# Performance work log

Measured on AMD Instinct MI355X. Metric: run time of the kernel, lower is better.

## Reference

```python
import jax, jax.numpy as jnp
import numpy as np

B, T, P = 4096, 128, 2
D_m = D_g = D_p = D_e = 256


def gru_cell(x, h, w_ih, w_hh, b_ih, b_hh):
    # PyTorch GRUCell math
    gi = x @ w_ih.T + b_ih          # [N, 3H]
    gh = h @ w_hh.T + b_hh          # [N, 3H]
    ir, iz, inn = jnp.split(gi, 3, axis=1)
    hr, hz, hn = jnp.split(gh, 3, axis=1)
    r = jax.nn.sigmoid(ir + hr)
    z = jax.nn.sigmoid(iz + hz)
    n = jnp.tanh(inn + r * hn)
    return (1.0 - z) * n + z * h


def _gru_params(key, in_dim, hid):
    k1, k2, k3, k4 = jax.random.split(key, 4)
    s = 1.0 / np.sqrt(hid)
    u = lambda k, shp: jax.random.uniform(k, shp, jnp.float32, -s, s)
    return u(k1, (3 * hid, in_dim)), u(k2, (3 * hid, hid)), u(k3, (3 * hid,)), u(k4, (3 * hid,))


def setup_inputs() -> dict:
    key = jax.random.key(0)
    ks = jax.random.split(key, 10)
    U = jax.random.normal(ks[0], (B, D_m), jnp.float32)
    qm_idx = jax.random.randint(ks[1], (B,), 0, P)
    g_hist = jax.random.normal(ks[2], (T, B, D_g), jnp.float32)
    q0 = jax.random.normal(ks[3], (B, P, D_p), jnp.float32)
    e0 = jax.random.normal(ks[4], (B, D_e), jnp.float32)
    wg = _gru_params(ks[5], D_m + D_p, D_g)
    wp = _gru_params(ks[6], D_m + D_g, D_p)
    we = _gru_params(ks[7], D_p, D_e)
    sa = 1.0 / np.sqrt(D_g)
    attn_w = jax.random.uniform(ks[8], (1, D_g), jnp.float32, -sa, sa)
    return {
        "U": U, "qm_idx": qm_idx, "g_hist": g_hist, "q0": q0, "e0": e0,
        "wg_ih": wg[0], "wg_hh": wg[1], "bg_ih": wg[2], "bg_hh": wg[3],
        "wp_ih": wp[0], "wp_hh": wp[1], "bp_ih": wp[2], "bp_hh": wp[3],
        "we_ih": we[0], "we_hh": we[1], "be_ih": we[2], "be_hh": we[3],
        "attn_w": attn_w,
    }


def reference(U, qm_idx, g_hist, q0, e0,
              wg_ih, wg_hh, bg_ih, bg_hh,
              wp_ih, wp_hh, bp_ih, bp_hh,
              we_ih, we_hh, be_ih, be_hh,
              attn_w):
    b_idx = jnp.arange(U.shape[0])
    qmask = jax.nn.one_hot(qm_idx, P, dtype=U.dtype)             # [B, P]
    # _select_parties: gather the speaking party's state
    q0_sel = q0[b_idx, qm_idx]                                    # [B, D_p]
    # global GRU step (g_hist non-empty -> hidden = g_hist[-1])
    g_ = gru_cell(jnp.concatenate([U, q0_sel], axis=1), g_hist[-1],
                  wg_ih, wg_hh, bg_ih, bg_hh)                     # [B, D_g]
    # SimpleAttention over history: softmax over time of a scalar score
    scale = jnp.einsum('tbd,od->tb', g_hist, attn_w)              # [T, B]
    alpha_t = jax.nn.softmax(scale, axis=0)                       # [T, B]
    c_ = jnp.einsum('tb,tbd->bd', alpha_t, g_hist)                # [B, D_g]
    alpha = alpha_t.T[:, None, :]                                 # [B, 1, T]
    # party GRU applied to every party slot
    U_c = jnp.concatenate([U, c_], axis=1)                        # [B, D_m+D_g]
    U_c_exp = jnp.broadcast_to(U_c[:, None, :], (U.shape[0], P, U_c.shape[1]))
    qs_ = gru_cell(U_c_exp.reshape(-1, D_m + D_g), q0.reshape(-1, D_p),
                   wp_ih, wp_hh, bp_ih, bp_hh).reshape(U.shape[0], P, D_p)
    # listener_state=False: listeners keep q0; speaker slot takes qs_
    qm = qmask[..., None]
    q_ = q0 * (1.0 - qm) + qs_ * qm                               # [B, P, D_p]
    # emotion GRU on the speaking party's updated state
    e_ = gru_cell(q_[b_idx, qm_idx], e0, we_ih, we_hh, be_ih, be_hh)  # [B, D_e]
    return g_, q_, e_, alpha
```

## Files before the change

### kernel.cpp

```cpp
#include <hip/hip_runtime.h>
#include <hip/hip_bf16.h>
#include <cstdint>
#include <cstddef>

#define B_N   4096
#define T_N   128
#define P_N   2
#define D     256
#define NG    768
#define BD    (B_N * D)
#define AGRID 1024
#define AGSIZE (AGRID * 256)

typedef __attribute__((ext_vector_type(4))) float f32x4;
typedef __attribute__((ext_vector_type(8))) short bf16x8;
typedef __attribute__((ext_vector_type(8))) unsigned short ushort8;

__device__ __forceinline__ unsigned short f2bf(float f) {
    __hip_bfloat16 h = __float2bfloat16(f);
    return *reinterpret_cast<unsigned short*>(&h);
}

struct AttnParams {
    const float *U, *g_hist, *q0, *e0;
    const int   *qm;
    const float *wg_ih, *wg_hh, *wp_ih, *wp_hh, *we_ih, *we_hh;
    const float *attn_w;
    float *a_out;
    unsigned short *U_bf, *e0_bf, *glast_bf, *q0sel_bf, *c_bf;
    unsigned short *wgih_bf, *wpih_bf, *wghh_bf, *wphh_bf, *weih_bf, *wehh_bf;
};

struct GPParams {
    const unsigned short *U_bf, *q0sel_bf, *glast_bf, *c_bf;
    const unsigned short *wgih_bf, *wghh_bf, *wpih_bf, *wphh_bf;
    const float *bg_ih, *bg_hh, *bp_ih, *bp_hh;
    const float *g_last, *q0;
    const int *qm;
    float *g_out, *q_out;
    unsigned short *qssel_bf;
};

__device__ __forceinline__ void cvt8(
    const float* __restrict__ src, unsigned short* __restrict__ dst,
    int n8, int gtid)
{
    for (int i = gtid; i < n8; i += AGSIZE) {
        const float4* s = reinterpret_cast<const float4*>(src + i * 8);
        const float4 v0 = s[0], v1 = s[1];
        ushort8 o = { f2bf(v0.x), f2bf(v0.y), f2bf(v0.z), f2bf(v0.w),
                      f2bf(v1.x), f2bf(v1.y), f2bf(v1.z), f2bf(v1.w) };
        *reinterpret_cast<ushort8*>(dst + i * 8) = o;
    }
}

__global__ __launch_bounds__(256) void attn_fused(AttnParams p)
{
    const int tid  = threadIdx.x;
    const int lane = tid & 63;
    const int wid  = tid >> 6;
    const int gtid = blockIdx.x * 256 + tid;

    const float* g_last = p.g_hist + (size_t)(T_N - 1) * BD;

    cvt8(p.wg_ih, p.wgih_bf, NG * 512 / 8, gtid);
    cvt8(p.wg_hh, p.wghh_bf, NG * 256 / 8, gtid);
    cvt8(p.wp_ih, p.wpih_bf, NG * 512 / 8, gtid);
    cvt8(p.wp_hh, p.wphh_bf, NG * 256 / 8, gtid);
    cvt8(p.we_ih, p.weih_bf, NG * 256 / 8, gtid);
    cvt8(p.we_hh, p.wehh_bf, NG * 256 / 8, gtid);
    cvt8(p.U,     p.U_bf,     B_N * D / 8, gtid);
    cvt8(p.e0,    p.e0_bf,    B_N * D / 8, gtid);
    cvt8(g_last,  p.glast_bf, B_N * D / 8, gtid);
    for (int i = gtid; i < B_N * D / 4; i += AGSIZE) {
        const int row = i >> 6;
        const int j   = (i & 63) * 4;
        const float4 v = *reinterpret_cast<const float4*>(
            p.q0 + ((size_t)row * P_N + p.qm[row]) * D + j);
        ushort4 bv = { f2bf(v.x), f2bf(v.y), f2bf(v.z), f2bf(v.w) };
        *reinterpret_cast<ushort4*>(p.q0sel_bf + (size_t)row * D + j) = bv;
    }

    const int b = blockIdx.x * 4 + wid;

    const float4 w4 = *reinterpret_cast<const float4*>(p.attn_w + lane * 4);
    const float* gbase = p.g_hist + (size_t)b * D + lane * 4;

    float  m = -INFINITY, l = 0.f;
    float4 acc = {0.f, 0.f, 0.f, 0.f};
    float  s0 = 0.f, s1 = 0.f;

    auto step = [&](int t, const float4& g) {
        float dot = g.x * w4.x + g.y * w4.y + g.z * w4.z + g.w * w4.w;
        #pragma unroll
        for (int off = 32; off >= 1; off >>= 1)
            dot += __shfl_xor(dot, off, 64);
        const float mn   = fmaxf(m, dot);
        const float corr = __expf(m - mn);
        const float pr   = __expf(dot - mn);
        l = l * corr + pr;
        acc.x = fmaf(pr, g.x, acc.x * corr);
        acc.y = fmaf(pr, g.y, acc.y * corr);
        acc.z = fmaf(pr, g.z, acc.z * corr);
        acc.w = fmaf(pr, g.w, acc.w * corr);
        m = mn;
        if ((t & 63) == lane) { if (t & 64) s1 = dot; else s0 = dot; }
    };

    for (int t = 0; t < T_N; t += 2) {
        const float4 g0 = *reinterpret_cast<const float4*>(gbase + (size_t)t * BD);
        const float4 g1 = *reinterpret_cast<const float4*>(gbase + (size_t)(t + 1) * BD);
        step(t, g0);
        step(t + 1, g1);
    }

    const float rl = 1.f / l;
    ushort4 cv = { f2bf(acc.x * rl), f2bf(acc.y * rl),
                   f2bf(acc.z * rl), f2bf(acc.w * rl) };
    *reinterpret_cast<ushort4*>(p.c_bf + (size_t)b * D + lane * 4) = cv;
    p.a_out[(size_t)b * T_N + lane]      = __expf(s0 - m) * rl;
    p.a_out[(size_t)b * T_N + 64 + lane] = __expf(s1 - m) * rl;
}

template<int MODE, int NI, int LDWI>
__device__ __forceinline__ void gru_body(
    int r0, int c0, unsigned short* smem, int tid,
    const unsigned short* __restrict__ A0,
    const unsigned short* __restrict__ A1,
    const unsigned short* __restrict__ Wi, const float* __restrict__ bi,
    const unsigned short* __restrict__ Ah,
    const unsigned short* __restrict__ Wh, const float* __restrict__ bh,
    const float* __restrict__ hsrc, const int* __restrict__ qm,
    float* __restrict__ out_f32, unsigned short* __restrict__ out_bf)
{
    constexpr int NT = NI + 8;

    const int lane = tid & 63;
    const int wid  = tid >> 6;
    const int st_row = lane >> 2;
    const int st_p   = lane & 3;

    f32x4 accI[2][6] = {};
    f32x4 accH[2][6] = {};

    auto stage = [&](int step, int buf) {
        const unsigned short* Apart;
        const unsigned short* W;
        int kcolA, kcolW, ldw;
        if (step < NI) {
            const int kt = step * 32;
            Apart = (kt < D) ? A0 : A1;
            kcolA = kt & (D - 1);
            kcolW = kt;
            W     = Wi;
            ldw   = LDWI;
        } else {
            const int kt = (step - NI) * 32;
            Apart = Ah; kcolA = kt; kcolW = kt; W = Wh; ldw = D;
        }
        unsigned short* As = smem + buf * 8192;
        unsigned short* Ws = As + 4096;
        #pragma unroll
        for (int c = 0; c < 2; ++c) {
            const int row  = wid * 32 + c * 16 + st_row;
            const int scol = (st_p ^ ((row >> 1) & 3)) * 8;
            __builtin_amdgcn_global_load_lds(
                (const __attribute__((address_space(1))) void*)
                    (Apart + (size_t)(r0 + row) * D + kcolA + scol),
                (__attribute__((address_space(3))) void*)
                    (As + wid * 1024 + c * 512), 16, 0, 0);
            int grp = row >> 5; if (grp == 3) grp = 2;
            const int wrow = grp * 256 + c0 + (row & 31);
            __builtin_amdgcn_global_load_lds(
                (const __attribute__((address_space(1))) void*)
                    (W + (size_t)wrow * ldw + kcolW + scol),
                (__attribute__((address_space(3))) void*)
                    (Ws + wid * 1024 + c * 512), 16, 0, 0);
        }
    };

    auto compute = [&](int buf, f32x4 (&acc)[2][6]) {
        const unsigned short* As = smem + buf * 8192;
        const unsigned short* Ws = As + 4096;
        const int s  = lane >> 4;
        const int fr = lane & 15;
        bf16x8 a[2], b[6];
        #pragma unroll
        for (int m = 0; m < 2; ++m) {
            const int row = wid * 32 + m * 16 + fr;
            const int ph  = s ^ ((row >> 1) & 3);
            a[m] = *reinterpret_cast<const bf16x8*>(&As[row * 32 + ph * 8]);
        }
        #pragma unroll
        for (int j = 0; j < 6; ++j) {
            const int row = j * 16 + fr;
            const int ph  = s ^ ((row >> 1) & 3);
            b[j] = *reinterpret_cast<const bf16x8*>(&Ws[row * 32 + ph * 8]);
        }
        #pragma unroll
        for (int m = 0; m < 2; ++m)
            #pragma unroll
            for (int j = 0; j < 6; ++j)
                acc[m][j] = __builtin_amdgcn_mfma_f32_16x16x32_bf16(
                    a[m], b[j], acc[m][j], 0, 0, 0);
    };

    stage(0, 0);
    stage(1, 1);

    int cb = 0, ib = 2;
    for (int s = 0; s < NT; ++s) {
        if (s + 2 < NT) stage(s + 2, ib);
        const int rem = NT - 1 - s;
        if (rem >= 2)      asm volatile("s_waitcnt vmcnt(8)" ::: "memory");
        else if (rem == 1) asm volatile("s_waitcnt vmcnt(4)" ::: "memory");
        else               asm volatile("s_waitcnt vmcnt(0)" ::: "memory");
        __builtin_amdgcn_sched_barrier(0);
        __builtin_amdgcn_s_barrier();
        if (s < NI) compute(cb, accI);
        else        compute(cb, accH);
        __builtin_amdgcn_s_barrier();
        cb = (cb == 2) ? 0 : cb + 1;
        ib = (ib == 2) ? 0 : ib + 1;
    }

    const int cr = (lane >> 4) * 4;
    const int cc = lane & 15;
    #pragma unroll
    for (int m = 0; m < 2; ++m) {
        #pragma unroll
        for (int jj = 0; jj < 2; ++jj) {
            const int col = c0 + jj * 16 + cc;
            const float bir = bi[col],       bhr = bh[col];
            const float biz = bi[col + 256], bhz = bh[col + 256];
            const float bin = bi[col + 512], bhn = bh[col + 512];
            #pragma unroll
            for (int q = 0; q < 4; ++q) {
                const int row = r0 + wid * 32 + m * 16 + cr + q;
                const float ir  = accI[m][jj][q]     + bir;
                const float hr  = accH[m][jj][q]     + bhr;
                const float iz  = accI[m][jj + 2][q] + biz;
                const float hz  = accH[m][jj + 2][q] + bhz;
                const float in_ = accI[m][jj + 4][q] + bin;
                const float hn  = accH[m][jj + 4][q] + bhn;
                const float rg = 1.f / (1.f + __expf(-(ir + hr)));
                const float zg = 1.f / (1.f + __expf(-(iz + hz)));
                const float ng = tanhf(in_ + rg * hn);
                if (MODE == 1) {
                    const int p = qm[row];
                    const float hv  = hsrc[(size_t)row * 512 + (size_t)p * 256 + col];
                    const float ov  = hsrc[(size_t)row * 512 + (size_t)(1 - p) * 256 + col];
                    const float val = (1.f - zg) * ng + zg * hv;
                    out_f32[(size_t)row * 512 + (size_t)p * 256 + col]       = val;
                    out_f32[(size_t)row * 512 + (size_t)(1 - p) * 256 + col] = ov;
                    out_bf[(size_t)row * 256 + col] = f2bf(val);
                } else {
                    const float hv  = hsrc[(size_t)row * 256 + col];
                    const float val = (1.f - zg) * ng + zg * hv;
                    out_f32[(size_t)row * 256 + col] = val;
                }
            }
        }
    }
}

__global__ __launch_bounds__(256) void gp_gru(GPParams p)
{
    __shared__ unsigned short smem[3 * 8192];
    const int tid = threadIdx.x;
    const int bid = blockIdx.x;

    if (bid < 256) {
        const int r0 = (bid & 31) * 128, c0 = (bid >> 5) * 32;
        gru_body<0, 16, 512>(r0, c0, smem, tid,
            p.U_bf, p.q0sel_bf, p.wgih_bf, p.bg_ih,
            p.glast_bf, p.wghh_bf, p.bg_hh,
            p.g_last, nullptr, p.g_out, nullptr);
    } else {
        const int gb = bid - 256;
        const int r0 = (gb & 31) * 128, c0 = (gb >> 5) * 32;
        gru_body<1, 16, 512>(r0, c0, smem, tid,
            p.U_bf, p.c_bf, p.wpih_bf, p.bp_ih,
            p.q0sel_bf, p.wphh_bf, p.bp_hh,
            p.q0, p.qm, p.q_out, p.qssel_bf);
    }
}

__global__ __launch_bounds__(256) void e_gru(
    const unsigned short* __restrict__ qssel_bf,
    const unsigned short* __restrict__ weih_bf, const float* __restrict__ be_ih,
    const unsigned short* __restrict__ e0_bf,
    const unsigned short* __restrict__ wehh_bf, const float* __restrict__ be_hh,
    const float* __restrict__ e0, float* __restrict__ e_out)
{
    __shared__ unsigned short smem[3 * 8192];
    const int tid = threadIdx.x;
    const int bid = blockIdx.x;
    const int r0 = (bid & 31) * 128, c0 = (bid >> 5) * 32;
    gru_body<0, 8, 256>(r0, c0, smem, tid,
        qssel_bf, nullptr, weih_bf, be_ih,
        e0_bf, wehh_bf, be_hh,
        e0, nullptr, e_out, nullptr);
}

extern "C" void kernel_launch(void* const* d_in, const int* in_sizes, int n_in,
                              void* d_out, int out_size, void* d_ws, size_t ws_size,
                              hipStream_t stream)
{
    const float* U      = (const float*)d_in[0];
    const int*   qm     = (const int*)  d_in[1];
    const float* g_hist = (const float*)d_in[2];
    const float* q0     = (const float*)d_in[3];
    const float* e0     = (const float*)d_in[4];
    const float* wg_ih  = (const float*)d_in[5];
    const float* wg_hh  = (const float*)d_in[6];
    const float* bg_ih  = (const float*)d_in[7];
    const float* bg_hh  = (const float*)d_in[8];
    const float* wp_ih  = (const float*)d_in[9];
    const float* wp_hh  = (const float*)d_in[10];
    const float* bp_ih  = (const float*)d_in[11];
    const float* bp_hh  = (const float*)d_in[12];
    const float* we_ih  = (const float*)d_in[13];
    const float* we_hh  = (const float*)d_in[14];
    const float* be_ih  = (const float*)d_in[15];
    const float* be_hh  = (const float*)d_in[16];
    const float* attn_w = (const float*)d_in[17];

    float* out   = (float*)d_out;
    float* g_out = out;
    float* q_out = out + 1048576;
    float* e_out = out + 3145728;
    float* a_out = out + 4194304;

    unsigned short* bf = (unsigned short*)d_ws;
    unsigned short* U_bf     = bf;
    unsigned short* e0_bf    = bf + 1048576;
    unsigned short* glast_bf = bf + 2097152;
    unsigned short* q0sel_bf = bf + 3145728;
    unsigned short* c_bf     = bf + 4194304;
    unsigned short* qssel_bf = bf + 5242880;
    unsigned short* wgih_bf  = bf + 6291456;
    unsigned short* wpih_bf  = bf + 6684672;
    unsigned short* wghh_bf  = bf + 7077888;
    unsigned short* wphh_bf  = bf + 7274496;
    unsigned short* weih_bf  = bf + 7471104;
    unsigned short* wehh_bf  = bf + 7667712;

    const float* g_last = g_hist + (size_t)(T_N - 1) * BD;

    AttnParams ap;
    ap.U = U; ap.g_hist = g_hist; ap.q0 = q0; ap.e0 = e0; ap.qm = qm;
    ap.wg_ih = wg_ih; ap.wg_hh = wg_hh; ap.wp_ih = wp_ih; ap.wp_hh = wp_hh;
    ap.we_ih = we_ih; ap.we_hh = we_hh; ap.attn_w = attn_w;
    ap.a_out = a_out;
    ap.U_bf = U_bf; ap.e0_bf = e0_bf; ap.glast_bf = glast_bf;
    ap.q0sel_bf = q0sel_bf; ap.c_bf = c_bf;
    ap.wgih_bf = wgih_bf; ap.wpih_bf = wpih_bf; ap.wghh_bf = wghh_bf;
    ap.wphh_bf = wphh_bf; ap.weih_bf = weih_bf; ap.wehh_bf = wehh_bf;

    GPParams gp;
    gp.U_bf = U_bf; gp.q0sel_bf = q0sel_bf; gp.glast_bf = glast_bf;
    gp.c_bf = c_bf;
    gp.wgih_bf = wgih_bf; gp.wghh_bf = wghh_bf;
    gp.wpih_bf = wpih_bf; gp.wphh_bf = wphh_bf;
    gp.bg_ih = bg_ih; gp.bg_hh = bg_hh; gp.bp_ih = bp_ih; gp.bp_hh = bp_hh;
    gp.g_last = g_last; gp.q0 = q0; gp.qm = qm;
    gp.g_out = g_out; gp.q_out = q_out; gp.qssel_bf = qssel_bf;

    const dim3 blk(256);
    attn_fused<<<AGRID, blk, 0, stream>>>(ap);
    gp_gru<<<512, blk, 0, stream>>>(gp);
    e_gru<<<256, blk, 0, stream>>>(
        qssel_bf, weih_bf, be_ih, e0_bf, wehh_bf, be_hh, e0, e_out);
}
```

Measured before the change: 162.0 us.

## Replace LDS-staged block GEMM with per-wave register-pipelined GRU tiles

The GRU GEMMs no longer stage A and W tiles through shared memory with block barriers. Each wave now independently computes a 16x32 output tile, loading its A and W fragments straight from global memory into registers with a 4-deep software pipeline. Grids are doubled so there are enough waves to cover the same output. Removing the barriers and LDS traffic trades away data reuse across waves: each W fragment is now fetched by many more waves, so more global/L2 traffic and register pressure.

```diff
diff --git a/kernel.cpp b/kernel.cpp
--- a/kernel.cpp
+++ b/kernel.cpp
@@ -123,8 +123,8 @@
 }
 
 template<int MODE, int NI, int LDWI>
-__device__ __forceinline__ void gru_body(
-    int r0, int c0, unsigned short* smem, int tid,
+__device__ __forceinline__ void gru_wave(
+    int row0, int c0, int lane,
     const unsigned short* __restrict__ A0,
     const unsigned short* __restrict__ A1,
     const unsigned short* __restrict__ Wi, const float* __restrict__ bi,
@@ -135,130 +135,93 @@
 {
     constexpr int NT = NI + 8;
 
-    const int lane = tid & 63;
-    const int wid  = tid >> 6;
-    const int st_row = lane >> 2;
-    const int st_p   = lane & 3;
-
-    f32x4 accI[2][6] = {};
-    f32x4 accH[2][6] = {};
-
-    auto stage = [&](int step, int buf) {
+    const int fr = lane & 15;
+    const int s  = lane >> 4;
+
+    f32x4 accI[6] = {};
+    f32x4 accH[6] = {};
+
+    bf16x8 a[4];
+    bf16x8 b[4][6];
+
+    auto loadstep = [&](int st, int buf) {
         const unsigned short* Apart;
         const unsigned short* W;
         int kcolA, kcolW, ldw;
-        if (step < NI) {
-            const int kt = step * 32;
+        if (st < NI) {
+            const int kt = st * 32;
             Apart = (kt < D) ? A0 : A1;
             kcolA = kt & (D - 1);
             kcolW = kt;
             W     = Wi;
             ldw   = LDWI;
         } else {
-            const int kt = (step - NI) * 32;
+            const int kt = (st - NI) * 32;
             Apart = Ah; kcolA = kt; kcolW = kt; W = Wh; ldw = D;
         }
-        unsigned short* As = smem + buf * 8192;
-        unsigned short* Ws = As + 4096;
+        a[buf] = *reinterpret_cast<const bf16x8*>(
+            Apart + (size_t)(row0 + fr) * D + kcolA + s * 8);
         #pragma unroll
-        for (int c = 0; c < 2; ++c) {
-            const int row  = wid * 32 + c * 16 + st_row;
-            const int scol = (st_p ^ ((row >> 1) & 3)) * 8;
-            __builtin_amdgcn_global_load_lds(
-                (const __attribute__((address_space(1))) void*)
-                    (Apart + (size_t)(r0 + row) * D + kcolA + scol),
-                (__attribute__((address_space(3))) void*)
-                    (As + wid * 1024 + c * 512), 16, 0, 0);
-            int grp = row >> 5; if (grp == 3) grp = 2;
-            const int wrow = grp * 256 + c0 + (row & 31);
-            __builtin_amdgcn_global_load_lds(
-                (const __attribute__((address_space(1))) void*)
-                    (W + (size_t)wrow * ldw + kcolW + scol),
-                (__attribute__((address_space(3))) void*)
-                    (Ws + wid * 1024 + c * 512), 16, 0, 0);
+        for (int j = 0; j < 6; ++j) {
+            const int wrow = (j >> 1) * 256 + c0 + (j & 1) * 16 + fr;
+            b[buf][j] = *reinterpret_cast<const bf16x8*>(
+                W + (size_t)wrow * ldw + kcolW + s * 8);
         }
     };
 
-    auto compute = [&](int buf, f32x4 (&acc)[2][6]) {
-        const unsigned short* As = smem + buf * 8192;
-        const unsigned short* Ws = As + 4096;
-        const int s  = lane >> 4;
-        const int fr = lane & 15;
-        bf16x8 a[2], b[6];
-        #pragma unroll
-        for (int m = 0; m < 2; ++m) {
-            const int row = wid * 32 + m * 16 + fr;
-            const int ph  = s ^ ((row >> 1) & 3);
-            a[m] = *reinterpret_cast<const bf16x8*>(&As[row * 32 + ph * 8]);
-        }
-        #pragma unroll
-        for (int j = 0; j < 6; ++j) {
-            const int row = j * 16 + fr;
-            const int ph  = s ^ ((row >> 1) & 3);
-            b[j] = *reinterpret_cast<const bf16x8*>(&Ws[row * 32 + ph * 8]);
-        }
-        #pragma unroll
-        for (int m = 0; m < 2; ++m)
+    loadstep(0, 0);
+    loadstep(1, 1);
+    loadstep(2, 2);
+
+    #pragma unroll
+    for (int st = 0; st < NT; ++st) {
+        if (st + 3 < NT) loadstep(st + 3, (st + 3) & 3);
+        const int buf = st & 3;
+        if (st < NI) {
             #pragma unroll
             for (int j = 0; j < 6; ++j)
-                acc[m][j] = __builtin_amdgcn_mfma_f32_16x16x32_bf16(
-                    a[m], b[j], acc[m][j], 0, 0, 0);
-    };
-
-    stage(0, 0);
-    stage(1, 1);
-
-    int cb = 0, ib = 2;
-    for (int s = 0; s < NT; ++s) {
-        if (s + 2 < NT) stage(s + 2, ib);
-        const int rem = NT - 1 - s;
-        if (rem >= 2)      asm volatile("s_waitcnt vmcnt(8)" ::: "memory");
-        else if (rem == 1) asm volatile("s_waitcnt vmcnt(4)" ::: "memory");
-        else               asm volatile("s_waitcnt vmcnt(0)" ::: "memory");
-        __builtin_amdgcn_sched_barrier(0);
-        __builtin_amdgcn_s_barrier();
-        if (s < NI) compute(cb, accI);
-        else        compute(cb, accH);
-        __builtin_amdgcn_s_barrier();
-        cb = (cb == 2) ? 0 : cb + 1;
-        ib = (ib == 2) ? 0 : ib + 1;
-    }
-
-    const int cr = (lane >> 4) * 4;
-    const int cc = lane & 15;
+                accI[j] = __builtin_amdgcn_mfma_f32_16x16x32_bf16(
+                    a[buf], b[buf][j], accI[j], 0, 0, 0);
+        } else {
+            #pragma unroll
+            for (int j = 0; j < 6; ++j)
+                accH[j] = __builtin_amdgcn_mfma_f32_16x16x32_bf16(
+                    a[buf], b[buf][j], accH[j], 0, 0, 0);
+        }
+    }
+
+    const int cr = s * 4;
+    const int cc = fr;
     #pragma unroll
-    for (int m = 0; m < 2; ++m) {
+    for (int jj = 0; jj < 2; ++jj) {
+        const int col = c0 + jj * 16 + cc;
+        const float bir = bi[col],       bhr = bh[col];
+        const float biz = bi[col + 256], bhz = bh[col + 256];
+        const float bin = bi[col + 512], bhn = bh[col + 512];
         #pragma unroll
-        for (int jj = 0; jj < 2; ++jj) {
-            const int col = c0 + jj * 16 + cc;
-            const float bir = bi[col],       bhr = bh[col];
-            const float biz = bi[col + 256], bhz = bh[col + 256];
-            const float bin = bi[col + 512], bhn = bh[col + 512];
-            #pragma unroll
-            for (int q = 0; q < 4; ++q) {
-                const int row = r0 + wid * 32 + m * 16 + cr + q;
-                const float ir  = accI[m][jj][q]     + bir;
-                const float hr  = accH[m][jj][q]     + bhr;
-                const float iz  = accI[m][jj + 2][q] + biz;
-                const float hz  = accH[m][jj + 2][q] + bhz;
-                const float in_ = accI[m][jj + 4][q] + bin;
-                const float hn  = accH[m][jj + 4][q] + bhn;
-                const float rg = 1.f / (1.f + __expf(-(ir + hr)));
-                const float zg = 1.f / (1.f + __expf(-(iz + hz)));
-                const float ng = tanhf(in_ + rg * hn);
-                if (MODE == 1) {
-                    const int p = qm[row];
-                    const float hv  = hsrc[(size_t)row * 512 + (size_t)p * 256 + col];
-                    const float ov  = hsrc[(size_t)row * 512 + (size_t)(1 - p) * 256 + col];
-                    const float val = (1.f - zg) * ng + zg * hv;
-                    out_f32[(size_t)row * 512 + (size_t)p * 256 + col]       = val;
-                    out_f32[(size_t)row * 512 + (size_t)(1 - p) * 256 + col] = ov;
-                    out_bf[(size_t)row * 256 + col] = f2bf(val);
-                } else {
-                    const float hv  = hsrc[(size_t)row * 256 + col];
-                    const float val = (1.f - zg) * ng + zg * hv;
-                    out_f32[(size_t)row * 256 + col] = val;
-                }
+        for (int q = 0; q < 4; ++q) {
+            const int row = row0 + cr + q;
+            const float ir  = accI[jj][q]     + bir;
+            const float hr  = accH[jj][q]     + bhr;
+            const float iz  = accI[jj + 2][q] + biz;
+            const float hz  = accH[jj + 2][q] + bhz;
+            const float in_ = accI[jj + 4][q] + bin;
+            const float hn  = accH[jj + 4][q] + bhn;
+            const float rg = 1.f / (1.f + __expf(-(ir + hr)));
+            const float zg = 1.f / (1.f + __expf(-(iz + hz)));
+            const float ng = tanhf(in_ + rg * hn);
+            if (MODE == 1) {
+                const int p = qm[row];
+                const float hv  = hsrc[(size_t)row * 512 + (size_t)p * 256 + col];
+                const float ov  = hsrc[(size_t)row * 512 + (size_t)(1 - p) * 256 + col];
+                const float val = (1.f - zg) * ng + zg * hv;
+                out_f32[(size_t)row * 512 + (size_t)p * 256 + col]       = val;
+                out_f32[(size_t)row * 512 + (size_t)(1 - p) * 256 + col] = ov;
+                out_bf[(size_t)row * 256 + col] = f2bf(val);
+            } else {
+                const float hv  = hsrc[(size_t)row * 256 + col];
+                const float val = (1.f - zg) * ng + zg * hv;
+                out_f32[(size_t)row * 256 + col] = val;
             }
         }
     }
@@ -266,20 +229,24 @@
 
 __global__ __launch_bounds__(256) void gp_gru(GPParams p)
 {
-    __shared__ unsigned short smem[3 * 8192];
-    const int tid = threadIdx.x;
-    const int bid = blockIdx.x;
-
-    if (bid < 256) {
-        const int r0 = (bid & 31) * 128, c0 = (bid >> 5) * 32;
-        gru_body<0, 16, 512>(r0, c0, smem, tid,
+    const int tid  = threadIdx.x;
+    const int lane = tid & 63;
+    const int wid  = tid >> 6;
+    const int bid  = blockIdx.x;
+
+    if (bid < 512) {
+        const int wg   = bid * 4 + wid;
+        const int row0 = (wg & 255) * 16;
+        const int c0   = (wg >> 8) * 32;
+        gru_wave<0, 16, 512>(row0, c0, lane,
             p.U_bf, p.q0sel_bf, p.wgih_bf, p.bg_ih,
             p.glast_bf, p.wghh_bf, p.bg_hh,
             p.g_last, nullptr, p.g_out, nullptr);
     } else {
-        const int gb = bid - 256;
-        const int r0 = (gb & 31) * 128, c0 = (gb >> 5) * 32;
-        gru_body<1, 16, 512>(r0, c0, smem, tid,
+        const int wg   = (bid - 512) * 4 + wid;
+        const int row0 = (wg & 255) * 16;
+        const int c0   = (wg >> 8) * 32;
+        gru_wave<1, 16, 512>(row0, c0, lane,
             p.U_bf, p.c_bf, p.wpih_bf, p.bp_ih,
             p.q0sel_bf, p.wphh_bf, p.bp_hh,
             p.q0, p.qm, p.q_out, p.qssel_bf);
@@ -293,11 +260,13 @@
     const unsigned short* __restrict__ wehh_bf, const float* __restrict__ be_hh,
     const float* __restrict__ e0, float* __restrict__ e_out)
 {
-    __shared__ unsigned short smem[3 * 8192];
-    const int tid = threadIdx.x;
-    const int bid = blockIdx.x;
-    const int r0 = (bid & 31) * 128, c0 = (bid >> 5) * 32;
-    gru_body<0, 8, 256>(r0, c0, smem, tid,
+    const int tid  = threadIdx.x;
+    const int lane = tid & 63;
+    const int wid  = tid >> 6;
+    const int wg   = blockIdx.x * 4 + wid;
+    const int row0 = (wg & 255) * 16;
+    const int c0   = (wg >> 8) * 32;
+    gru_wave<0, 8, 256>(row0, c0, lane,
         qssel_bf, nullptr, weih_bf, be_ih,
         e0_bf, wehh_bf, be_hh,
         e0, nullptr, e_out, nullptr);
@@ -369,7 +338,7 @@
 
     const dim3 blk(256);
     attn_fused<<<AGRID, blk, 0, stream>>>(ap);
-    gp_gru<<<512, blk, 0, stream>>>(gp);
-    e_gru<<<256, blk, 0, stream>>>(
+    gp_gru<<<1024, blk, 0, stream>>>(gp);
+    e_gru<<<512, blk, 0, stream>>>(
         qssel_bf, weih_bf, be_ih, e0_bf, wehh_bf, be_hh, e0, e_out);
 }
```

Measured after the change: 221.7 us. 36.8% more time.

## Overlap global GRU with attention, split conversion kernel, use 64-row GRU tiles

Applied to the files above, without the earlier changes.

Conversion of weights and activations moves into its own kernel. The global GRU, which does not depend on the attention context, now runs inside the attention kernel as every fifth block, using a simple synchronous 128-row tile so its matmul overlaps the memory-bound attention scan. The party and emotion GRUs switch to 64-row tiles with twice as many blocks to raise occupancy. The cost is one extra kernel launch and a non-pipelined GRU path for the global cell.

```diff
diff --git a/kernel.cpp b/kernel.cpp
--- a/kernel.cpp
+++ b/kernel.cpp
@@ -9,8 +9,8 @@
 #define D     256
 #define NG    768
 #define BD    (B_N * D)
-#define AGRID 1024
-#define AGSIZE (AGRID * 256)
+#define CGRID 1024
+#define CGSIZE (CGRID * 256)
 
 typedef __attribute__((ext_vector_type(4))) float f32x4;
 typedef __attribute__((ext_vector_type(8))) short bf16x8;
@@ -21,31 +21,27 @@
     return *reinterpret_cast<unsigned short*>(&h);
 }
 
-struct AttnParams {
-    const float *U, *g_hist, *q0, *e0;
+struct CvtParams {
+    const float *U, *e0, *g_last, *q0;
     const int   *qm;
     const float *wg_ih, *wg_hh, *wp_ih, *wp_hh, *we_ih, *we_hh;
-    const float *attn_w;
-    float *a_out;
-    unsigned short *U_bf, *e0_bf, *glast_bf, *q0sel_bf, *c_bf;
+    unsigned short *U_bf, *e0_bf, *glast_bf, *q0sel_bf;
     unsigned short *wgih_bf, *wpih_bf, *wghh_bf, *wphh_bf, *weih_bf, *wehh_bf;
 };
 
-struct GPParams {
-    const unsigned short *U_bf, *q0sel_bf, *glast_bf, *c_bf;
-    const unsigned short *wgih_bf, *wghh_bf, *wpih_bf, *wphh_bf;
-    const float *bg_ih, *bg_hh, *bp_ih, *bp_hh;
-    const float *g_last, *q0;
-    const int *qm;
-    float *g_out, *q_out;
-    unsigned short *qssel_bf;
+struct AttnGParams {
+    const float *g_hist, *attn_w, *g_last;
+    float *a_out, *g_out;
+    unsigned short *c_bf;
+    const unsigned short *U_bf, *q0sel_bf, *glast_bf, *wgih_bf, *wghh_bf;
+    const float *bg_ih, *bg_hh;
 };
 
 __device__ __forceinline__ void cvt8(
     const float* __restrict__ src, unsigned short* __restrict__ dst,
     int n8, int gtid)
 {
-    for (int i = gtid; i < n8; i += AGSIZE) {
+    for (int i = gtid; i < n8; i += CGSIZE) {
         const float4* s = reinterpret_cast<const float4*>(src + i * 8);
         const float4 v0 = s[0], v1 = s[1];
         ushort8 o = { f2bf(v0.x), f2bf(v0.y), f2bf(v0.z), f2bf(v0.w),
@@ -54,25 +50,19 @@
     }
 }
 
-__global__ __launch_bounds__(256) void attn_fused(AttnParams p)
-{
-    const int tid  = threadIdx.x;
-    const int lane = tid & 63;
-    const int wid  = tid >> 6;
-    const int gtid = blockIdx.x * 256 + tid;
-
-    const float* g_last = p.g_hist + (size_t)(T_N - 1) * BD;
-
+__global__ __launch_bounds__(256) void cvt_all(CvtParams p)
+{
+    const int gtid = blockIdx.x * 256 + threadIdx.x;
     cvt8(p.wg_ih, p.wgih_bf, NG * 512 / 8, gtid);
     cvt8(p.wg_hh, p.wghh_bf, NG * 256 / 8, gtid);
     cvt8(p.wp_ih, p.wpih_bf, NG * 512 / 8, gtid);
     cvt8(p.wp_hh, p.wphh_bf, NG * 256 / 8, gtid);
     cvt8(p.we_ih, p.weih_bf, NG * 256 / 8, gtid);
     cvt8(p.we_hh, p.wehh_bf, NG * 256 / 8, gtid);
-    cvt8(p.U,     p.U_bf,     B_N * D / 8, gtid);
-    cvt8(p.e0,    p.e0_bf,    B_N * D / 8, gtid);
-    cvt8(g_last,  p.glast_bf, B_N * D / 8, gtid);
-    for (int i = gtid; i < B_N * D / 4; i += AGSIZE) {
+    cvt8(p.U,      p.U_bf,     B_N * D / 8, gtid);
+    cvt8(p.e0,     p.e0_bf,    B_N * D / 8, gtid);
+    cvt8(p.g_last, p.glast_bf, B_N * D / 8, gtid);
+    for (int i = gtid; i < B_N * D / 4; i += CGSIZE) {
         const int row = i >> 6;
         const int j   = (i & 63) * 4;
         const float4 v = *reinterpret_cast<const float4*>(
@@ -80,61 +70,18 @@
         ushort4 bv = { f2bf(v.x), f2bf(v.y), f2bf(v.z), f2bf(v.w) };
         *reinterpret_cast<ushort4*>(p.q0sel_bf + (size_t)row * D + j) = bv;
     }
-
-    const int b = blockIdx.x * 4 + wid;
-
-    const float4 w4 = *reinterpret_cast<const float4*>(p.attn_w + lane * 4);
-    const float* gbase = p.g_hist + (size_t)b * D + lane * 4;
-
-    float  m = -INFINITY, l = 0.f;
-    float4 acc = {0.f, 0.f, 0.f, 0.f};
-    float  s0 = 0.f, s1 = 0.f;
-
-    auto step = [&](int t, const float4& g) {
-        float dot = g.x * w4.x + g.y * w4.y + g.z * w4.z + g.w * w4.w;
-        #pragma unroll
-        for (int off = 32; off >= 1; off >>= 1)
-            dot += __shfl_xor(dot, off, 64);
-        const float mn   = fmaxf(m, dot);
-        const float corr = __expf(m - mn);
-        const float pr   = __expf(dot - mn);
-        l = l * corr + pr;
-        acc.x = fmaf(pr, g.x, acc.x * corr);
-        acc.y = fmaf(pr, g.y, acc.y * corr);
-        acc.z = fmaf(pr, g.z, acc.z * corr);
-        acc.w = fmaf(pr, g.w, acc.w * corr);
-        m = mn;
-        if ((t & 63) == lane) { if (t & 64) s1 = dot; else s0 = dot; }
-    };
-
-    for (int t = 0; t < T_N; t += 2) {
-        const float4 g0 = *reinterpret_cast<const float4*>(gbase + (size_t)t * BD);
-        const float4 g1 = *reinterpret_cast<const float4*>(gbase + (size_t)(t + 1) * BD);
-        step(t, g0);
-        step(t + 1, g1);
-    }
-
-    const float rl = 1.f / l;
-    ushort4 cv = { f2bf(acc.x * rl), f2bf(acc.y * rl),
-                   f2bf(acc.z * rl), f2bf(acc.w * rl) };
-    *reinterpret_cast<ushort4*>(p.c_bf + (size_t)b * D + lane * 4) = cv;
-    p.a_out[(size_t)b * T_N + lane]      = __expf(s0 - m) * rl;
-    p.a_out[(size_t)b * T_N + 64 + lane] = __expf(s1 - m) * rl;
-}
-
-template<int MODE, int NI, int LDWI>
-__device__ __forceinline__ void gru_body(
-    int r0, int c0, unsigned short* smem, int tid,
+}
+
+template<int NI, int LDWI>
+__device__ __forceinline__ void gru_sync128(
+    int r0, int c0, unsigned short* As, unsigned short* Ws, int tid,
     const unsigned short* __restrict__ A0,
     const unsigned short* __restrict__ A1,
     const unsigned short* __restrict__ Wi, const float* __restrict__ bi,
     const unsigned short* __restrict__ Ah,
     const unsigned short* __restrict__ Wh, const float* __restrict__ bh,
-    const float* __restrict__ hsrc, const int* __restrict__ qm,
-    float* __restrict__ out_f32, unsigned short* __restrict__ out_bf)
-{
-    constexpr int NT = NI + 8;
-
+    const float* __restrict__ hsrc, float* __restrict__ out_f32)
+{
     const int lane = tid & 63;
     const int wid  = tid >> 6;
     const int st_row = lane >> 2;
@@ -143,23 +90,8 @@
     f32x4 accI[2][6] = {};
     f32x4 accH[2][6] = {};
 
-    auto stage = [&](int step, int buf) {
-        const unsigned short* Apart;
-        const unsigned short* W;
-        int kcolA, kcolW, ldw;
-        if (step < NI) {
-            const int kt = step * 32;
-            Apart = (kt < D) ? A0 : A1;
-            kcolA = kt & (D - 1);
-            kcolW = kt;
-            W     = Wi;
-            ldw   = LDWI;
-        } else {
-            const int kt = (step - NI) * 32;
-            Apart = Ah; kcolA = kt; kcolW = kt; W = Wh; ldw = D;
-        }
-        unsigned short* As = smem + buf * 8192;
-        unsigned short* Ws = As + 4096;
+    auto kstep = [&](const unsigned short* Apart, int kcolA, int kcolW,
+                     const unsigned short* W, int ldw, f32x4 (&acc)[2][6]) {
         #pragma unroll
         for (int c = 0; c < 2; ++c) {
             const int row  = wid * 32 + c * 16 + st_row;
@@ -177,11 +109,8 @@
                 (__attribute__((address_space(3))) void*)
                     (Ws + wid * 1024 + c * 512), 16, 0, 0);
         }
-    };
-
-    auto compute = [&](int buf, f32x4 (&acc)[2][6]) {
-        const unsigned short* As = smem + buf * 8192;
-        const unsigned short* Ws = As + 4096;
+        __syncthreads();
+
         const int s  = lane >> 4;
         const int fr = lane & 15;
         bf16x8 a[2], b[6];
@@ -203,26 +132,15 @@
             for (int j = 0; j < 6; ++j)
                 acc[m][j] = __builtin_amdgcn_mfma_f32_16x16x32_bf16(
                     a[m], b[j], acc[m][j], 0, 0, 0);
+        __syncthreads();
     };
 
-    stage(0, 0);
-    stage(1, 1);
-
-    int cb = 0, ib = 2;
-    for (int s = 0; s < NT; ++s) {
-        if (s + 2 < NT) stage(s + 2, ib);
-        const int rem = NT - 1 - s;
-        if (rem >= 2)      asm volatile("s_waitcnt vmcnt(8)" ::: "memory");
-        else if (rem == 1) asm volatile("s_waitcnt vmcnt(4)" ::: "memory");
-        else               asm volatile("s_waitcnt vmcnt(0)" ::: "memory");
-        __builtin_amdgcn_sched_barrier(0);
-        __builtin_amdgcn_s_barrier();
-        if (s < NI) compute(cb, accI);
-        else        compute(cb, accH);
-        __builtin_amdgcn_s_barrier();
-        cb = (cb == 2) ? 0 : cb + 1;
-        ib = (ib == 2) ? 0 : ib + 1;
-    }
+    for (int kt = 0; kt < NI * 32; kt += 32) {
+        const unsigned short* Ap = (kt < D) ? A0 : A1;
+        kstep(Ap, kt & (D - 1), kt, Wi, LDWI, accI);
+    }
+    for (int kt = 0; kt < D; kt += 32)
+        kstep(Ah, kt, kt, Wh, D, accH);
 
     const int cr = (lane >> 4) * 4;
     const int cc = lane & 15;
@@ -246,44 +164,235 @@
                 const float rg = 1.f / (1.f + __expf(-(ir + hr)));
                 const float zg = 1.f / (1.f + __expf(-(iz + hz)));
                 const float ng = tanhf(in_ + rg * hn);
-                if (MODE == 1) {
-                    const int p = qm[row];
-                    const float hv  = hsrc[(size_t)row * 512 + (size_t)p * 256 + col];
-                    const float ov  = hsrc[(size_t)row * 512 + (size_t)(1 - p) * 256 + col];
-                    const float val = (1.f - zg) * ng + zg * hv;
-                    out_f32[(size_t)row * 512 + (size_t)p * 256 + col]       = val;
-                    out_f32[(size_t)row * 512 + (size_t)(1 - p) * 256 + col] = ov;
-                    out_bf[(size_t)row * 256 + col] = f2bf(val);
-                } else {
-                    const float hv  = hsrc[(size_t)row * 256 + col];
-                    const float val = (1.f - zg) * ng + zg * hv;
-                    out_f32[(size_t)row * 256 + col] = val;
-                }
+                const float hv  = hsrc[(size_t)row * 256 + col];
+                out_f32[(size_t)row * 256 + col] = (1.f - zg) * ng + zg * hv;
             }
         }
     }
 }
 
-__global__ __launch_bounds__(256) void gp_gru(GPParams p)
-{
-    __shared__ unsigned short smem[3 * 8192];
-    const int tid = threadIdx.x;
-    const int bid = blockIdx.x;
-
-    if (bid < 256) {
-        const int r0 = (bid & 31) * 128, c0 = (bid >> 5) * 32;
-        gru_body<0, 16, 512>(r0, c0, smem, tid,
+__global__ __launch_bounds__(256) void attn_g(AttnGParams p)
+{
+    __shared__ unsigned short As[128 * 32];
+    __shared__ unsigned short Ws[128 * 32];
+
+    const int tid  = threadIdx.x;
+    const int lane = tid & 63;
+    const int wid  = tid >> 6;
+    const int bid  = blockIdx.x;
+    const int g5   = bid / 5;
+    const int r5   = bid - g5 * 5;
+
+    if (r5 == 4) {
+        const int r0 = (g5 & 31) * 128, c0 = (g5 >> 5) * 32;
+        gru_sync128<16, 512>(r0, c0, As, Ws, tid,
             p.U_bf, p.q0sel_bf, p.wgih_bf, p.bg_ih,
             p.glast_bf, p.wghh_bf, p.bg_hh,
-            p.g_last, nullptr, p.g_out, nullptr);
-    } else {
-        const int gb = bid - 256;
-        const int r0 = (gb & 31) * 128, c0 = (gb >> 5) * 32;
-        gru_body<1, 16, 512>(r0, c0, smem, tid,
-            p.U_bf, p.c_bf, p.wpih_bf, p.bp_ih,
-            p.q0sel_bf, p.wphh_bf, p.bp_hh,
-            p.q0, p.qm, p.q_out, p.qssel_bf);
-    }
+            p.g_last, p.g_out);
+        return;
+    }
+
+    const int b = (g5 * 4 + r5) * 4 + wid;
+
+    const float4 w4 = *reinterpret_cast<const float4*>(p.attn_w + lane * 4);
+    const float* gbase = p.g_hist + (size_t)b * D + lane * 4;
+
+    float  m = -INFINITY, l = 0.f;
+    float4 acc = {0.f, 0.f, 0.f, 0.f};
+    float  s0 = 0.f, s1 = 0.f;
+
+    auto step = [&](int t, const float4& g) {
+        float dot = g.x * w4.x + g.y * w4.y + g.z * w4.z + g.w * w4.w;
+        #pragma unroll
+        for (int off = 32; off >= 1; off >>= 1)
+            dot += __shfl_xor(dot, off, 64);
+        const float mn   = fmaxf(m, dot);
+        const float corr = __expf(m - mn);
+        const float pr   = __expf(dot - mn);
+        l = l * corr + pr;
+        acc.x = fmaf(pr, g.x, acc.x * corr);
+        acc.y = fmaf(pr, g.y, acc.y * corr);
+        acc.z = fmaf(pr, g.z, acc.z * corr);
+        acc.w = fmaf(pr, g.w, acc.w * corr);
+        m = mn;
+        if ((t & 63) == lane) { if (t & 64) s1 = dot; else s0 = dot; }
+    };
+
+    for (int t = 0; t < T_N; t += 2) {
+        const float4 g0 = *reinterpret_cast<const float4*>(gbase + (size_t)t * BD);
+        const float4 g1 = *reinterpret_cast<const float4*>(gbase + (size_t)(t + 1) * BD);
+        step(t, g0);
+        step(t + 1, g1);
+    }
+
+    const float rl = 1.f / l;
+    ushort4 cv = { f2bf(acc.x * rl), f2bf(acc.y * rl),
+                   f2bf(acc.z * rl), f2bf(acc.w * rl) };
+    *reinterpret_cast<ushort4*>(p.c_bf + (size_t)b * D + lane * 4) = cv;
+    p.a_out[(size_t)b * T_N + lane]      = __expf(s0 - m) * rl;
+    p.a_out[(size_t)b * T_N + 64 + lane] = __expf(s1 - m) * rl;
+}
+
+template<int MODE, int NI, int LDWI>
+__device__ __forceinline__ void gru_body64(
+    int r0, int c0, unsigned short* smem, int tid,
+    const unsigned short* __restrict__ A0,
+    const unsigned short* __restrict__ A1,
+    const unsigned short* __restrict__ Wi, const float* __restrict__ bi,
+    const unsigned short* __restrict__ Ah,
+    const unsigned short* __restrict__ Wh, const float* __restrict__ bh,
+    const float* __restrict__ hsrc, const int* __restrict__ qm,
+    float* __restrict__ out_f32, unsigned short* __restrict__ out_bf)
+{
+    constexpr int NT = NI + 8;
+
+    const int lane = tid & 63;
+    const int wid  = tid >> 6;
+    const int st_row = lane >> 2;
+    const int st_p   = lane & 3;
+
+    f32x4 accI[6] = {};
+    f32x4 accH[6] = {};
+
+    auto stage = [&](int step, int buf) {
+        const unsigned short* Apart;
+        const unsigned short* W;
+        int kcolA, kcolW, ldw;
+        if (step < NI) {
+            const int kt = step * 32;
+            Apart = (kt < D) ? A0 : A1;
+            kcolA = kt & (D - 1);
+            kcolW = kt;
+            W     = Wi;
+            ldw   = LDWI;
+        } else {
+            const int kt = (step - NI) * 32;
+            Apart = Ah; kcolA = kt; kcolW = kt; W = Wh; ldw = D;
+        }
+        unsigned short* As = smem + buf * 6144;
+        unsigned short* Ws = As + 2048;
+        {
+            const int row  = wid * 16 + st_row;
+            const int scol = (st_p ^ ((row >> 1) & 3)) * 8;
+            __builtin_amdgcn_global_load_lds(
+                (const __attribute__((address_space(1))) void*)
+                    (Apart + (size_t)(r0 + row) * D + kcolA + scol),
+                (__attribute__((address_space(3))) void*)
+                    (As + wid * 512), 16, 0, 0);
+        }
+        #pragma unroll
+        for (int c = 0; c < 2; ++c) {
+            const int row  = wid * 32 + c * 16 + st_row;
+            const int scol = (st_p ^ ((row >> 1) & 3)) * 8;
+            int grp = row >> 5; if (grp == 3) grp = 2;
+            const int wrow = grp * 256 + c0 + (row & 31);
+            __builtin_amdgcn_global_load_lds(
+                (const __attribute__((address_space(1))) void*)
+                    (W + (size_t)wrow * ldw + kcolW + scol),
+                (__attribute__((address_space(3))) void*)
+                    (Ws + wid * 1024 + c * 512), 16, 0, 0);
+        }
+    };
+
+    auto compute = [&](int buf, f32x4 (&acc)[6]) {
+        const unsigned short* As = smem + buf * 6144;
+        const unsigned short* Ws = As + 2048;
+        const int s  = lane >> 4;
+        const int fr = lane & 15;
+        bf16x8 a, b[6];
+        {
+            const int row = wid * 16 + fr;
+            const int ph  = s ^ ((row >> 1) & 3);
+            a = *reinterpret_cast<const bf16x8*>(&As[row * 32 + ph * 8]);
+        }
+        #pragma unroll
+        for (int j = 0; j < 6; ++j) {
+            const int row = j * 16 + fr;
+            const int ph  = s ^ ((row >> 1) & 3);
+            b[j] = *reinterpret_cast<const bf16x8*>(&Ws[row * 32 + ph * 8]);
+        }
+        #pragma unroll
+        for (int j = 0; j < 6; ++j)
+            acc[j] = __builtin_amdgcn_mfma_f32_16x16x32_bf16(
+                a, b[j], acc[j], 0, 0, 0);
+    };
+
+    asm volatile("s_waitcnt vmcnt(0)" ::: "memory");
+    __builtin_amdgcn_sched_barrier(0);
+
+    stage(0, 0);
+    stage(1, 1);
+
+    int cb = 0, ib = 2;
+    for (int s = 0; s < NT; ++s) {
+        if (s + 2 < NT) stage(s + 2, ib);
+        const int rem = NT - 1 - s;
+        if (rem >= 2)      asm volatile("s_waitcnt vmcnt(6)" ::: "memory");
+        else if (rem == 1) asm volatile("s_waitcnt vmcnt(3)" ::: "memory");
+        else               asm volatile("s_waitcnt vmcnt(0)" ::: "memory");
+        __builtin_amdgcn_sched_barrier(0);
+        __builtin_amdgcn_s_barrier();
+        if (s < NI) compute(cb, accI);
+        else        compute(cb, accH);
+        __builtin_amdgcn_s_barrier();
+        cb = (cb == 2) ? 0 : cb + 1;
+        ib = (ib == 2) ? 0 : ib + 1;
+    }
+    __builtin_amdgcn_sched_barrier(0);
+
+    const int cr = (lane >> 4) * 4;
+    const int cc = lane & 15;
+    #pragma unroll
+    for (int jj = 0; jj < 2; ++jj) {
+        const int col = c0 + jj * 16 + cc;
+        const float bir = bi[col],       bhr = bh[col];
+        const float biz = bi[col + 256], bhz = bh[col + 256];
+        const float bin = bi[col + 512], bhn = bh[col + 512];
+        #pragma unroll
+        for (int q = 0; q < 4; ++q) {
+            const int row = r0 + wid * 16 + cr + q;
+            const float ir  = accI[jj][q]     + bir;
+            const float hr  = accH[jj][q]     + bhr;
+            const float iz  = accI[jj + 2][q] + biz;
+            const float hz  = accH[jj + 2][q] + bhz;
+            const float in_ = accI[jj + 4][q] + bin;
+            const float hn  = accH[jj + 4][q] + bhn;
+            const float rg = 1.f / (1.f + __expf(-(ir + hr)));
+            const float zg = 1.f / (1.f + __expf(-(iz + hz)));
+            const float ng = tanhf(in_ + rg * hn);
+            if (MODE == 1) {
+                const int p = qm[row];
+                const float hv  = hsrc[(size_t)row * 512 + (size_t)p * 256 + col];
+                const float ov  = hsrc[(size_t)row * 512 + (size_t)(1 - p) * 256 + col];
+                const float val = (1.f - zg) * ng + zg * hv;
+                out_f32[(size_t)row * 512 + (size_t)p * 256 + col]       = val;
+                out_f32[(size_t)row * 512 + (size_t)(1 - p) * 256 + col] = ov;
+                out_bf[(size_t)row * 256 + col] = f2bf(val);
+            } else {
+                const float hv  = hsrc[(size_t)row * 256 + col];
+                const float val = (1.f - zg) * ng + zg * hv;
+                out_f32[(size_t)row * 256 + col] = val;
+            }
+        }
+    }
+}
+
+__global__ __launch_bounds__(256) void party_gru(
+    const unsigned short* __restrict__ U_bf,
+    const unsigned short* __restrict__ c_bf,
+    const unsigned short* __restrict__ wpih_bf, const float* __restrict__ bp_ih,
+    const unsigned short* __restrict__ q0sel_bf,
+    const unsigned short* __restrict__ wphh_bf, const float* __restrict__ bp_hh,
+    const float* __restrict__ q0, const int* __restrict__ qm,
+    float* __restrict__ q_out, unsigned short* __restrict__ qssel_bf)
+{
+    __shared__ unsigned short smem[3 * 6144];
+    const int bid = blockIdx.x;
+    const int r0 = (bid & 63) * 64, c0 = (bid >> 6) * 32;
+    gru_body64<1, 16, 512>(r0, c0, smem, threadIdx.x,
+        U_bf, c_bf, wpih_bf, bp_ih,
+        q0sel_bf, wphh_bf, bp_hh,
+        q0, qm, q_out, qssel_bf);
 }
 
 __global__ __launch_bounds__(256) void e_gru(
@@ -293,11 +402,10 @@
     const unsigned short* __restrict__ wehh_bf, const float* __restrict__ be_hh,
     const float* __restrict__ e0, float* __restrict__ e_out)
 {
-    __shared__ unsigned short smem[3 * 8192];
-    const int tid = threadIdx.x;
+    __shared__ unsigned short smem[3 * 6144];
     const int bid = blockIdx.x;
-    const int r0 = (bid & 31) * 128, c0 = (bid >> 5) * 32;
-    gru_body<0, 8, 256>(r0, c0, smem, tid,
+    const int r0 = (bid & 63) * 64, c0 = (bid >> 6) * 32;
+    gru_body64<0, 8, 256>(r0, c0, smem, threadIdx.x,
         qssel_bf, nullptr, weih_bf, be_ih,
         e0_bf, wehh_bf, be_hh,
         e0, nullptr, e_out, nullptr);
@@ -348,28 +456,28 @@
 
     const float* g_last = g_hist + (size_t)(T_N - 1) * BD;
 
-    AttnParams ap;
-    ap.U = U; ap.g_hist = g_hist; ap.q0 = q0; ap.e0 = e0; ap.qm = qm;
-    ap.wg_ih = wg_ih; ap.wg_hh = wg_hh; ap.wp_ih = wp_ih; ap.wp_hh = wp_hh;
-    ap.we_ih = we_ih; ap.we_hh = we_hh; ap.attn_w = attn_w;
-    ap.a_out = a_out;
-    ap.U_bf = U_bf; ap.e0_bf = e0_bf; ap.glast_bf = glast_bf;
-    ap.q0sel_bf = q0sel_bf; ap.c_bf = c_bf;
-    ap.wgih_bf = wgih_bf; ap.wpih_bf = wpih_bf; ap.wghh_bf = wghh_bf;
-    ap.wphh_bf = wphh_bf; ap.weih_bf = weih_bf; ap.wehh_bf = wehh_bf;
-
-    GPParams gp;
-    gp.U_bf = U_bf; gp.q0sel_bf = q0sel_bf; gp.glast_bf = glast_bf;
-    gp.c_bf = c_bf;
-    gp.wgih_bf = wgih_bf; gp.wghh_bf = wghh_bf;
-    gp.wpih_bf = wpih_bf; gp.wphh_bf = wphh_bf;
-    gp.bg_ih = bg_ih; gp.bg_hh = bg_hh; gp.bp_ih = bp_ih; gp.bp_hh = bp_hh;
-    gp.g_last = g_last; gp.q0 = q0; gp.qm = qm;
-    gp.g_out = g_out; gp.q_out = q_out; gp.qssel_bf = qssel_bf;
+    CvtParams cp;
+    cp.U = U; cp.e0 = e0; cp.g_last = g_last; cp.q0 = q0; cp.qm = qm;
+    cp.wg_ih = wg_ih; cp.wg_hh = wg_hh; cp.wp_ih = wp_ih; cp.wp_hh = wp_hh;
+    cp.we_ih = we_ih; cp.we_hh = we_hh;
+    cp.U_bf = U_bf; cp.e0_bf = e0_bf; cp.glast_bf = glast_bf;
+    cp.q0sel_bf = q0sel_bf;
+    cp.wgih_bf = wgih_bf; cp.wpih_bf = wpih_bf; cp.wghh_bf = wghh_bf;
+    cp.wphh_bf = wphh_bf; cp.weih_bf = weih_bf; cp.wehh_bf = wehh_bf;
+
+    AttnGParams ag;
+    ag.g_hist = g_hist; ag.attn_w = attn_w; ag.g_last = g_last;
+    ag.a_out = a_out; ag.g_out = g_out; ag.c_bf = c_bf;
+    ag.U_bf = U_bf; ag.q0sel_bf = q0sel_bf; ag.glast_bf = glast_bf;
+    ag.wgih_bf = wgih_bf; ag.wghh_bf = wghh_bf;
+    ag.bg_ih = bg_ih; ag.bg_hh = bg_hh;
 
     const dim3 blk(256);
-    attn_fused<<<AGRID, blk, 0, stream>>>(ap);
-    gp_gru<<<512, blk, 0, stream>>>(gp);
-    e_gru<<<256, blk, 0, stream>>>(
+    cvt_all<<<CGRID, blk, 0, stream>>>(cp);
+    attn_g<<<1280, blk, 0, stream>>>(ag);
+    party_gru<<<512, blk, 0, stream>>>(
+        U_bf, c_bf, wpih_bf, bp_ih, q0sel_bf, wphh_bf, bp_hh,
+        q0, qm, q_out, qssel_bf);
+    e_gru<<<512, blk, 0, stream>>>(
         qssel_bf, weih_bf, be_ih, e0_bf, wehh_bf, be_hh, e0, e_out);
 }
```

Result: slower. 215.2 us (+32.8%).

## Switch GRU GEMM to 64-wide K tiles with double buffering; unroll attention loop by four

Applied to the files above, without the earlier changes.

The GRU GEMM body now stages 64-column K slices instead of 32, using two 32 KB LDS buffers in place of three 16 KB ones, with a new XOR swizzle over 8 chunks. This halves the number of barrier-separated pipeline steps. Staging for the next-but-one step is issued after the compute barrier rather than before the wait. The attention scan also loads four timesteps per iteration instead of two, to keep more loads in flight. The trade-off is higher LDS use per block (64 KB vs 48 KB), which may reduce occupancy, and one fewer buffer of prefetch depth.

```diff
diff --git a/kernel.cpp b/kernel.cpp
--- a/kernel.cpp
+++ b/kernel.cpp
@@ -107,11 +107,15 @@
         if ((t & 63) == lane) { if (t & 64) s1 = dot; else s0 = dot; }
     };
 
-    for (int t = 0; t < T_N; t += 2) {
-        const float4 g0 = *reinterpret_cast<const float4*>(gbase + (size_t)t * BD);
-        const float4 g1 = *reinterpret_cast<const float4*>(gbase + (size_t)(t + 1) * BD);
-        step(t, g0);
-        step(t + 1, g1);
+    for (int t = 0; t < T_N; t += 4) {
+        const float4 ga = *reinterpret_cast<const float4*>(gbase + (size_t)t * BD);
+        const float4 gb = *reinterpret_cast<const float4*>(gbase + (size_t)(t + 1) * BD);
+        const float4 gc = *reinterpret_cast<const float4*>(gbase + (size_t)(t + 2) * BD);
+        const float4 gd = *reinterpret_cast<const float4*>(gbase + (size_t)(t + 3) * BD);
+        step(t,     ga);
+        step(t + 1, gb);
+        step(t + 2, gc);
+        step(t + 3, gd);
     }
 
     const float rl = 1.f / l;
@@ -122,8 +126,8 @@
     p.a_out[(size_t)b * T_N + 64 + lane] = __expf(s1 - m) * rl;
 }
 
-template<int MODE, int NI, int LDWI>
-__device__ __forceinline__ void gru_body(
+template<int MODE, int NI64, int LDWI>
+__device__ __forceinline__ void gru_body_k64(
     int r0, int c0, unsigned short* smem, int tid,
     const unsigned short* __restrict__ A0,
     const unsigned short* __restrict__ A1,
@@ -133,12 +137,12 @@
     const float* __restrict__ hsrc, const int* __restrict__ qm,
     float* __restrict__ out_f32, unsigned short* __restrict__ out_bf)
 {
-    constexpr int NT = NI + 8;
+    constexpr int NT = NI64 + 4;
 
     const int lane = tid & 63;
     const int wid  = tid >> 6;
-    const int st_row = lane >> 2;
-    const int st_p   = lane & 3;
+    const int st_row = lane >> 3;
+    const int st_p   = lane & 7;
 
     f32x4 accI[2][6] = {};
     f32x4 accH[2][6] = {};
@@ -147,82 +151,85 @@
         const unsigned short* Apart;
         const unsigned short* W;
         int kcolA, kcolW, ldw;
-        if (step < NI) {
-            const int kt = step * 32;
+        if (step < NI64) {
+            const int kt = step * 64;
             Apart = (kt < D) ? A0 : A1;
             kcolA = kt & (D - 1);
             kcolW = kt;
             W     = Wi;
             ldw   = LDWI;
         } else {
-            const int kt = (step - NI) * 32;
+            const int kt = (step - NI64) * 64;
             Apart = Ah; kcolA = kt; kcolW = kt; W = Wh; ldw = D;
         }
-        unsigned short* As = smem + buf * 8192;
-        unsigned short* Ws = As + 4096;
+        unsigned short* As = smem + buf * 16384;
+        unsigned short* Ws = As + 8192;
         #pragma unroll
-        for (int c = 0; c < 2; ++c) {
-            const int row  = wid * 32 + c * 16 + st_row;
-            const int scol = (st_p ^ ((row >> 1) & 3)) * 8;
+        for (int c = 0; c < 4; ++c) {
+            const int row  = wid * 32 + c * 8 + st_row;
+            const int scol = (st_p ^ (row & 7)) * 8;
             __builtin_amdgcn_global_load_lds(
                 (const __attribute__((address_space(1))) void*)
                     (Apart + (size_t)(r0 + row) * D + kcolA + scol),
                 (__attribute__((address_space(3))) void*)
-                    (As + wid * 1024 + c * 512), 16, 0, 0);
+                    (As + (wid * 32 + c * 8) * 64), 16, 0, 0);
             int grp = row >> 5; if (grp == 3) grp = 2;
             const int wrow = grp * 256 + c0 + (row & 31);
             __builtin_amdgcn_global_load_lds(
                 (const __attribute__((address_space(1))) void*)
                     (W + (size_t)wrow * ldw + kcolW + scol),
                 (__attribute__((address_space(3))) void*)
-                    (Ws + wid * 1024 + c * 512), 16, 0, 0);
+                    (Ws + (wid * 32 + c * 8) * 64), 16, 0, 0);
         }
     };
 
     auto compute = [&](int buf, f32x4 (&acc)[2][6]) {
-        const unsigned short* As = smem + buf * 8192;
-        const unsigned short* Ws = As + 4096;
+        const unsigned short* As = smem + buf * 16384;
+        const unsigned short* Ws = As + 8192;
         const int s  = lane >> 4;
         const int fr = lane & 15;
-        bf16x8 a[2], b[6];
         #pragma unroll
-        for (int m = 0; m < 2; ++m) {
-            const int row = wid * 32 + m * 16 + fr;
-            const int ph  = s ^ ((row >> 1) & 3);
-            a[m] = *reinterpret_cast<const bf16x8*>(&As[row * 32 + ph * 8]);
+        for (int kap = 0; kap < 2; ++kap) {
+            const int sl = kap * 4 + s;
+            bf16x8 a[2], b[6];
+            #pragma unroll
+            for (int m = 0; m < 2; ++m) {
+                const int row = wid * 32 + m * 16 + fr;
+                const int ph  = sl ^ (row & 7);
+                a[m] = *reinterpret_cast<const bf16x8*>(&As[row * 64 + ph * 8]);
+            }
+            #pragma unroll
+            for (int j = 0; j < 6; ++j) {
+                const int row = j * 16 + fr;
+                const int ph  = sl ^ (row & 7);
+                b[j] = *reinterpret_cast<const bf16x8*>(&Ws[row * 64 + ph * 8]);
+            }
+            #pragma unroll
+            for (int m = 0; m < 2; ++m)
+                #pragma unroll
+                for (int j = 0; j < 6; ++j)
+                    acc[m][j] = __builtin_amdgcn_mfma_f32_16x16x32_bf16(
+                        a[m], b[j], acc[m][j], 0, 0, 0);
         }
-        #pragma unroll
-        for (int j = 0; j < 6; ++j) {
-            const int row = j * 16 + fr;
-            const int ph  = s ^ ((row >> 1) & 3);
-            b[j] = *reinterpret_cast<const bf16x8*>(&Ws[row * 32 + ph * 8]);
-        }
-        #pragma unroll
-        for (int m = 0; m < 2; ++m)
-            #pragma unroll
-            for (int j = 0; j < 6; ++j)
-                acc[m][j] = __builtin_amdgcn_mfma_f32_16x16x32_bf16(
-                    a[m], b[j], acc[m][j], 0, 0, 0);
     };
+
+    asm volatile("s_waitcnt vmcnt(0)" ::: "memory");
+    __builtin_amdgcn_sched_barrier(0);
 
     stage(0, 0);
     stage(1, 1);
 
-    int cb = 0, ib = 2;
-    for (int s = 0; s < NT; ++s) {
-        if (s + 2 < NT) stage(s + 2, ib);
-        const int rem = NT - 1 - s;
-        if (rem >= 2)      asm volatile("s_waitcnt vmcnt(8)" ::: "memory");
-        else if (rem == 1) asm volatile("s_waitcnt vmcnt(4)" ::: "memory");
-        else               asm volatile("s_waitcnt vmcnt(0)" ::: "memory");
+    for (int st = 0; st < NT; ++st) {
+        if (st + 1 < NT) asm volatile("s_waitcnt vmcnt(8)" ::: "memory");
+        else             asm volatile("s_waitcnt vmcnt(0)" ::: "memory");
         __builtin_amdgcn_sched_barrier(0);
         __builtin_amdgcn_s_barrier();
-        if (s < NI) compute(cb, accI);
-        else        compute(cb, accH);
+        if (st < NI64) compute(st & 1, accI);
+        else           compute(st & 1, accH);
         __builtin_amdgcn_s_barrier();
-        cb = (cb == 2) ? 0 : cb + 1;
-        ib = (ib == 2) ? 0 : ib + 1;
-    }
+        if (st + 2 < NT) stage(st + 2, st & 1);
+    }
+    __builtin_amdgcn_sched_barrier(0);
 
     const int cr = (lane >> 4) * 4;
     const int cc = lane & 15;
@@ -266,20 +273,20 @@
 
 __global__ __launch_bounds__(256) void gp_gru(GPParams p)
 {
-    __shared__ unsigned short smem[3 * 8192];
+    __shared__ unsigned short smem[2 * 16384];
     const int tid = threadIdx.x;
     const int bid = blockIdx.x;
 
     if (bid < 256) {
         const int r0 = (bid & 31) * 128, c0 = (bid >> 5) * 32;
-        gru_body<0, 16, 512>(r0, c0, smem, tid,
+        gru_body_k64<0, 8, 512>(r0, c0, smem, tid,
             p.U_bf, p.q0sel_bf, p.wgih_bf, p.bg_ih,
             p.glast_bf, p.wghh_bf, p.bg_hh,
             p.g_last, nullptr, p.g_out, nullptr);
     } else {
         const int gb = bid - 256;
         const int r0 = (gb & 31) * 128, c0 = (gb >> 5) * 32;
-        gru_body<1, 16, 512>(r0, c0, smem, tid,
+        gru_body_k64<1, 8, 512>(r0, c0, smem, tid,
             p.U_bf, p.c_bf, p.wpih_bf, p.bp_ih,
             p.q0sel_bf, p.wphh_bf, p.bp_hh,
             p.q0, p.qm, p.q_out, p.qssel_bf);
@@ -293,11 +300,11 @@
     const unsigned short* __restrict__ wehh_bf, const float* __restrict__ be_hh,
     const float* __restrict__ e0, float* __restrict__ e_out)
 {
-    __shared__ unsigned short smem[3 * 8192];
+    __shared__ unsigned short smem[2 * 16384];
     const int tid = threadIdx.x;
     const int bid = blockIdx.x;
     const int r0 = (bid & 31) * 128, c0 = (bid >> 5) * 32;
-    gru_body<0, 8, 256>(r0, c0, smem, tid,
+    gru_body_k64<0, 4, 256>(r0, c0, smem, tid,
         qssel_bf, nullptr, weih_bf, be_ih,
         e0_bf, wehh_bf, be_hh,
         e0, nullptr, e_out, nullptr);
```

New measurement: 164.4 us. No clear change (+1.5%).
